# Kernel optimization log

Measured on AMD Instinct MI355X. Metric: run time of the kernel, lower is better.

The kernel has to match this reference:

```python
import jax, jax.numpy as jnp
import numpy as np

BATCH = 512          # bs_large + bs_small
COMBINED_BS = 320    # bs_large + bs_small // (r_large // r_small)
R = 64               # r_large
K = 4096             # hidden dim, fixed in the TIR kernel
N_ADAPT = 80         # combined adapters


def setup_inputs() -> dict:
    key = jax.random.key(0)
    k1, k2, k3, k4 = jax.random.split(key, 4)
    x = jax.random.normal(k1, (BATCH, 1, K), dtype=jnp.float32)
    xids = jax.random.randint(k2, (COMBINED_BS * R,), 0, BATCH, dtype=jnp.int32)
    wids = jax.random.randint(k3, (COMBINED_BS,), 0, N_ADAPT, dtype=jnp.int32)
    A = jax.random.normal(k4, (N_ADAPT, K, R), dtype=jnp.float32) * 0.02
    return {"x": x, "xids": xids, "wids": wids, "A": A}


def reference(x, xids, wids, A):
    # out[c, 0, r] = sum_k x[xids[c*R + r], 0, k] * A[wids[c], k, r]
    C = wids.shape[0]
    r = A.shape[2]
    tok = xids.reshape(C, r)          # per-output-element token ids
    xg = x[tok, 0, :]                 # (C, R, K) gathered activations
    Ag = A[wids]                      # (C, K, R) gathered adapters
    out = jnp.einsum('crk,ckr->cr', xg, Ag)
    return out[:, None, :]            # (C, 1, R)
```

## Files before the change

### kernel.cpp

```cpp
#include <hip/hip_runtime.h>

namespace {
constexpr int CBS   = 320;
constexpr int R     = 64;
constexpr int K     = 4096;
constexpr int SPLIT = 8;
constexpr int KS    = K / SPLIT;
constexpr int TK    = 64;
constexpr int NT    = 256;
constexpr int NW    = NT / 64;
constexpr int NTILES = KS / TK;
}

__global__ __launch_bounds__(NT)
void lora_a_kernel(const float* __restrict__ x,
                   const int*   __restrict__ xids,
                   const int*   __restrict__ wids,
                   const float* __restrict__ A,
                   float*       __restrict__ out)
{
    __shared__ float xs[TK * R];
    __shared__ float red[NW * R];

    const int bid  = blockIdx.x;
    const int c    = bid >> 3;
    const int s    = bid & 7;
    const int t    = threadIdx.x;
    const int wave = t >> 6;
    const int lane = t & 63;
    const int r4   = lane & 15;
    const int kq   = lane >> 4;

    const int wid = wids[c];
    const float* __restrict__ Aw = A + (size_t)wid * (K * R);

    const int rw  = t >> 2;
    const int jq  = t & 3;
    const int tok = xids[c * R + rw];
    const float* __restrict__ xrow = x + (size_t)tok * K + s * KS + jq * 16;

    float4 acc = make_float4(0.f, 0.f, 0.f, 0.f);

    float4 pv[4];
    {
        const float4* src = (const float4*)xrow;
#pragma unroll
        for (int ii = 0; ii < 4; ++ii) pv[ii] = src[ii];
    }

    for (int tile = 0; tile < NTILES; ++tile) {
#pragma unroll
        for (int ii = 0; ii < 4; ++ii) {
            const int kk = jq * 16 + ii * 4;
            xs[(kk + 0) * R + rw] = pv[ii].x;
            xs[(kk + 1) * R + rw] = pv[ii].y;
            xs[(kk + 2) * R + rw] = pv[ii].z;
            xs[(kk + 3) * R + rw] = pv[ii].w;
        }
        __syncthreads();

        if (tile + 1 < NTILES) {
            const float4* src = (const float4*)(xrow + (tile + 1) * TK);
#pragma unroll
            for (int ii = 0; ii < 4; ++ii) pv[ii] = src[ii];
        }

        const int kw = wave * 16 + kq;
        const float* __restrict__ Ap =
            Aw + (size_t)(s * KS + tile * TK + kw) * R + 4 * r4;
#pragma unroll
        for (int i = 0; i < 4; ++i) {
            float4 av = *(const float4*)(Ap + (size_t)(4 * i) * R);
            float4 xv = *(const float4*)(&xs[(kw + 4 * i) * R + 4 * r4]);
            acc.x = fmaf(xv.x, av.x, acc.x);
            acc.y = fmaf(xv.y, av.y, acc.y);
            acc.z = fmaf(xv.z, av.z, acc.z);
            acc.w = fmaf(xv.w, av.w, acc.w);
        }
        __syncthreads();
    }

#pragma unroll
    for (int m = 16; m < 64; m <<= 1) {
        acc.x += __shfl_xor(acc.x, m, 64);
        acc.y += __shfl_xor(acc.y, m, 64);
        acc.z += __shfl_xor(acc.z, m, 64);
        acc.w += __shfl_xor(acc.w, m, 64);
    }
    if (kq == 0) {
        float* rd = &red[wave * R + 4 * r4];
        rd[0] = acc.x; rd[1] = acc.y; rd[2] = acc.z; rd[3] = acc.w;
    }
    __syncthreads();

    if (wave == 0) {
        float sum = red[lane] + red[R + lane] + red[2 * R + lane] + red[3 * R + lane];
        atomicAdd(&out[c * R + lane], sum);
    }
}

extern "C" void kernel_launch(void* const* d_in, const int* in_sizes, int n_in,
                              void* d_out, int out_size, void* d_ws, size_t ws_size,
                              hipStream_t stream)
{
    (void)in_sizes; (void)n_in; (void)d_ws; (void)ws_size;
    const float* x    = (const float*)d_in[0];
    const int*   xids = (const int*)d_in[1];
    const int*   wids = (const int*)d_in[2];
    const float* A    = (const float*)d_in[3];
    float* out        = (float*)d_out;

    hipMemsetAsync(out, 0, (size_t)out_size * sizeof(float), stream);

    hipLaunchKernelGGL(lora_a_kernel, dim3(CBS * SPLIT), dim3(NT), 0, stream,
                       x, xids, wids, A, out);
}
```

Before: 156.0 us.

## Convert x to bf16 in workspace, sort chunks by adapter, swizzle LDS

Adds a pre-pass that converts x to bf16 in the workspace, which halves the bytes of the gathered activation rows read by the main kernel. A single-block counting sort orders the chunks by adapter id so that blocks sharing an adapter run close together, improving cache reuse of A. The LDS transpose store and the reads now use an XOR swizzle to cut bank conflicts. This rounds x to bf16, which loses accuracy, and adds two extra kernel launches and a full read/write pass over x; an fp32 fallback kernel is kept for when the workspace is too small.

```diff
diff --git a/kernel.cpp b/kernel.cpp
--- a/kernel.cpp
+++ b/kernel.cpp
@@ -1,19 +1,151 @@
 #include <hip/hip_runtime.h>
+#include <stdint.h>
 
 namespace {
-constexpr int CBS   = 320;
-constexpr int R     = 64;
-constexpr int K     = 4096;
-constexpr int SPLIT = 8;
-constexpr int KS    = K / SPLIT;
-constexpr int TK    = 64;
-constexpr int NT    = 256;
-constexpr int NW    = NT / 64;
+constexpr int BATCH  = 512;
+constexpr int CBS    = 320;
+constexpr int R      = 64;
+constexpr int K      = 4096;
+constexpr int NADAPT = 80;
+constexpr int SPLIT  = 8;
+constexpr int KS     = K / SPLIT;
+constexpr int TK     = 64;
+constexpr int NT     = 256;
+constexpr int NW     = NT / 64;
 constexpr int NTILES = KS / TK;
+
+constexpr size_t WS_X_OFF  = 4096;
+constexpr size_t WS_NEEDED = WS_X_OFF + (size_t)BATCH * K * 2;
+
+__device__ inline uint16_t f2bf(float f) {
+    uint32_t u = __float_as_uint(f);
+    u += 0x7fffu + ((u >> 16) & 1u);
+    return (uint16_t)(u >> 16);
+}
+__device__ inline float bf2f(uint16_t b) {
+    return __uint_as_float((uint32_t)b << 16);
+}
+}
+
+__global__ void sort_by_wid(const int* __restrict__ wids, int* __restrict__ perm)
+{
+    __shared__ int hist[NADAPT];
+    __shared__ int offs[NADAPT];
+    const int t = threadIdx.x;
+    if (t < NADAPT) hist[t] = 0;
+    __syncthreads();
+    atomicAdd(&hist[wids[t]], 1);
+    __syncthreads();
+    if (t == 0) {
+        int run = 0;
+        for (int i = 0; i < NADAPT; ++i) { offs[i] = run; run += hist[i]; }
+    }
+    __syncthreads();
+    const int pos = atomicAdd(&offs[wids[t]], 1);
+    perm[pos] = t;
+}
+
+__global__ __launch_bounds__(256)
+void cvt_x(const float* __restrict__ x, uint16_t* __restrict__ xb)
+{
+    const int i = blockIdx.x * 256 + threadIdx.x;
+    const float4 v = ((const float4*)x)[i];
+    ushort4 o;
+    o.x = f2bf(v.x); o.y = f2bf(v.y); o.z = f2bf(v.z); o.w = f2bf(v.w);
+    ((ushort4*)xb)[i] = o;
 }
 
 __global__ __launch_bounds__(NT)
-void lora_a_kernel(const float* __restrict__ x,
+void lora_main(const int* __restrict__ xids,
+               const int* __restrict__ wids,
+               const float* __restrict__ A,
+               const uint16_t* __restrict__ xb,
+               const int* __restrict__ perm,
+               float* __restrict__ out)
+{
+    __shared__ float xs[TK * R];
+    __shared__ float red[NW * R];
+
+    const int bid  = blockIdx.x;
+    const int i0   = bid >> 3;
+    const int s    = bid & 7;
+    const int c    = perm[i0];
+    const int t    = threadIdx.x;
+    const int wave = t >> 6;
+    const int lane = t & 63;
+    const int r4   = lane & 15;
+    const int kq   = lane >> 4;
+
+    const int wid = wids[c];
+    const float* __restrict__ Aw = A + (size_t)wid * (K * R);
+
+    const int rw  = t >> 2;
+    const int jq  = t & 3;
+    const int tok = xids[c * R + rw];
+    const uint16_t* __restrict__ xrow = xb + (size_t)tok * K + s * KS + jq * 16;
+    const int rsw = rw ^ (jq * 16);
+
+    float4 acc = make_float4(0.f, 0.f, 0.f, 0.f);
+
+    uint4 p0, p1;
+    {
+        const uint4* src = (const uint4*)xrow;
+        p0 = src[0]; p1 = src[1];
+    }
+
+    for (int tile = 0; tile < NTILES; ++tile) {
+        {
+            const uint32_t w[8] = {p0.x, p0.y, p0.z, p0.w, p1.x, p1.y, p1.z, p1.w};
+            float* base = xs + (jq * 16) * R + rsw;
+#pragma unroll
+            for (int m = 0; m < 8; ++m) {
+                base[(2 * m + 0) * R] = bf2f((uint16_t)(w[m] & 0xffffu));
+                base[(2 * m + 1) * R] = bf2f((uint16_t)(w[m] >> 16));
+            }
+        }
+        __syncthreads();
+
+        if (tile + 1 < NTILES) {
+            const uint4* src = (const uint4*)(xrow + (tile + 1) * TK);
+            p0 = src[0]; p1 = src[1];
+        }
+
+        const int kw = wave * 16 + kq;
+        const int rr = (4 * r4) ^ (wave * 16);
+        const float* __restrict__ Ap =
+            Aw + (size_t)(s * KS + tile * TK + kw) * R + 4 * r4;
+#pragma unroll
+        for (int i = 0; i < 4; ++i) {
+            float4 av = *(const float4*)(Ap + (size_t)(4 * i) * R);
+            float4 xv = *(const float4*)(&xs[(kw + 4 * i) * R + rr]);
+            acc.x = fmaf(xv.x, av.x, acc.x);
+            acc.y = fmaf(xv.y, av.y, acc.y);
+            acc.z = fmaf(xv.z, av.z, acc.z);
+            acc.w = fmaf(xv.w, av.w, acc.w);
+        }
+        __syncthreads();
+    }
+
+#pragma unroll
+    for (int m = 16; m < 64; m <<= 1) {
+        acc.x += __shfl_xor(acc.x, m, 64);
+        acc.y += __shfl_xor(acc.y, m, 64);
+        acc.z += __shfl_xor(acc.z, m, 64);
+        acc.w += __shfl_xor(acc.w, m, 64);
+    }
+    if (kq == 0) {
+        float* rd = &red[wave * R + 4 * r4];
+        rd[0] = acc.x; rd[1] = acc.y; rd[2] = acc.z; rd[3] = acc.w;
+    }
+    __syncthreads();
+    if (wave == 0) {
+        float sum = red[lane] + red[R + lane] + red[2 * R + lane] + red[3 * R + lane];
+        atomicAdd(&out[c * R + lane], sum);
+    }
+}
+
+__global__ __launch_bounds__(NT)
+void lora_fallback(const float* __restrict__ x,
                    const int*   __restrict__ xids,
                    const int*   __restrict__ wids,
                    const float* __restrict__ A,
@@ -21,7 +153,6 @@
 {
     __shared__ float xs[TK * R];
     __shared__ float red[NW * R];
-
     const int bid  = blockIdx.x;
     const int c    = bid >> 3;
     const int s    = bid & 7;
@@ -30,24 +161,19 @@
     const int lane = t & 63;
     const int r4   = lane & 15;
     const int kq   = lane >> 4;
-
-    const int wid = wids[c];
+    const int wid  = wids[c];
     const float* __restrict__ Aw = A + (size_t)wid * (K * R);
-
     const int rw  = t >> 2;
     const int jq  = t & 3;
     const int tok = xids[c * R + rw];
     const float* __restrict__ xrow = x + (size_t)tok * K + s * KS + jq * 16;
-
     float4 acc = make_float4(0.f, 0.f, 0.f, 0.f);
-
     float4 pv[4];
     {
         const float4* src = (const float4*)xrow;
 #pragma unroll
         for (int ii = 0; ii < 4; ++ii) pv[ii] = src[ii];
     }
-
     for (int tile = 0; tile < NTILES; ++tile) {
 #pragma unroll
         for (int ii = 0; ii < 4; ++ii) {
@@ -58,13 +184,11 @@
             xs[(kk + 3) * R + rw] = pv[ii].w;
         }
         __syncthreads();
-
         if (tile + 1 < NTILES) {
             const float4* src = (const float4*)(xrow + (tile + 1) * TK);
 #pragma unroll
             for (int ii = 0; ii < 4; ++ii) pv[ii] = src[ii];
         }
-
         const int kw = wave * 16 + kq;
         const float* __restrict__ Ap =
             Aw + (size_t)(s * KS + tile * TK + kw) * R + 4 * r4;
@@ -79,7 +203,6 @@
         }
         __syncthreads();
     }
-
 #pragma unroll
     for (int m = 16; m < 64; m <<= 1) {
         acc.x += __shfl_xor(acc.x, m, 64);
@@ -92,7 +215,6 @@
         rd[0] = acc.x; rd[1] = acc.y; rd[2] = acc.z; rd[3] = acc.w;
     }
     __syncthreads();
-
     if (wave == 0) {
         float sum = red[lane] + red[R + lane] + red[2 * R + lane] + red[3 * R + lane];
         atomicAdd(&out[c * R + lane], sum);
@@ -103,7 +225,7 @@
                               void* d_out, int out_size, void* d_ws, size_t ws_size,
                               hipStream_t stream)
 {
-    (void)in_sizes; (void)n_in; (void)d_ws; (void)ws_size;
+    (void)in_sizes; (void)n_in;
     const float* x    = (const float*)d_in[0];
     const int*   xids = (const int*)d_in[1];
     const int*   wids = (const int*)d_in[2];
@@ -112,6 +234,15 @@
 
     hipMemsetAsync(out, 0, (size_t)out_size * sizeof(float), stream);
 
-    hipLaunchKernelGGL(lora_a_kernel, dim3(CBS * SPLIT), dim3(NT), 0, stream,
-                       x, xids, wids, A, out);
-}
+    if (ws_size >= WS_NEEDED) {
+        int*      perm = (int*)d_ws;
+        uint16_t* xb   = (uint16_t*)((char*)d_ws + WS_X_OFF);
+        hipLaunchKernelGGL(sort_by_wid, dim3(1), dim3(CBS), 0, stream, wids, perm);
+        hipLaunchKernelGGL(cvt_x, dim3(BATCH * K / 4 / 256), dim3(256), 0, stream, x, xb);
+        hipLaunchKernelGGL(lora_main, dim3(CBS * SPLIT), dim3(NT), 0, stream,
+                           xids, wids, A, xb, perm, out);
+    } else {
+        hipLaunchKernelGGL(lora_fallback, dim3(CBS * SPLIT), dim3(NT), 0, stream,
+                           x, xids, wids, A, out);
+    }
+}
```

Result: faster. 147.7 us (-5.3%).
